# Kernel optimization log

Measured on AMD Instinct MI355X. Metric: run time of the kernel, lower is better.

Reference implementation:

```python
import jax, jax.numpy as jnp
import numpy as np

D_MODEL = 1024
D_CTRL = 1024
N_HEADS = 16
TOPK = 4
TEMPERATURE = 1.0
LN_EPS = 1e-5


def layer_norm(x, g, b):
    m = jnp.mean(x, axis=-1, keepdims=True)
    v = jnp.mean(jnp.square(x - m), axis=-1, keepdims=True)
    return (x - m) * jax.lax.rsqrt(v + LN_EPS) * g + b


def setup_inputs() -> dict:
    key = jax.random.key(0)
    ks = jax.random.split(key, 8)
    B, S = 8, 2048
    s = 0.02
    return {
        "x": jax.random.normal(ks[0], (B, S, D_MODEL), dtype=jnp.float32),
        "state": jnp.zeros((B, D_CTRL), dtype=jnp.float32),
        # pool LayerNorm
        "pool_g": jnp.ones((D_MODEL,), jnp.float32),
        "pool_b": jnp.zeros((D_MODEL,), jnp.float32),
        # inp_proj
        "inp_w": jax.random.normal(ks[1], (D_MODEL, D_CTRL), jnp.float32) * s,
        "inp_b": jnp.zeros((D_CTRL,), jnp.float32),
        # W_z, W_h
        "wz_w": jax.random.normal(ks[2], (D_CTRL, D_CTRL), jnp.float32) * s,
        "wz_b": jnp.zeros((D_CTRL,), jnp.float32),
        "wh_w": jax.random.normal(ks[3], (D_CTRL, D_CTRL), jnp.float32) * s,
        "wh_b": jnp.zeros((D_CTRL,), jnp.float32),
        # ln_h
        "lnh_g": jnp.ones((D_CTRL,), jnp.float32),
        "lnh_b": jnp.zeros((D_CTRL,), jnp.float32),
        # router: LayerNorm(d_model+d_ctrl) -> Linear -> GELU -> Linear
        "rln_g": jnp.ones((D_MODEL + D_CTRL,), jnp.float32),
        "rln_b": jnp.zeros((D_MODEL + D_CTRL,), jnp.float32),
        "r_w1": jax.random.normal(ks[4], (D_MODEL + D_CTRL, D_CTRL), jnp.float32) * s,
        "r_b1": jnp.zeros((D_CTRL,), jnp.float32),
        "r_w2": jax.random.normal(ks[5], (D_CTRL, N_HEADS), jnp.float32) * s,
        "r_b2": jnp.zeros((N_HEADS,), jnp.float32),
    }


def reference(x, state, pool_g, pool_b, inp_w, inp_b, wz_w, wz_b, wh_w, wh_b,
              lnh_g, lnh_b, rln_g, rln_b, r_w1, r_b1, r_w2, r_b2):
    B, S, D = x.shape
    # pool: LayerNorm over tokens then mean over sequence -> [B, d_model]
    g = jnp.mean(layer_norm(x, pool_g, pool_b), axis=1)
    x_ctrl = g @ inp_w + inp_b  # [B, d_ctrl]
    z = jax.nn.sigmoid(x_ctrl @ wz_w + wz_b)
    h_cand = jnp.tanh(x_ctrl @ wh_w + wh_b)
    h_new = (1.0 - z) * state + z * h_cand
    h_new = layer_norm(h_new, lnh_g, lnh_b)  # [B, d_ctrl]
    # token-conditioned router on concat([X, h_tok])
    h_tok = jnp.broadcast_to(h_new[:, None, :], (B, S, D_CTRL))
    cat = jnp.concatenate([x, h_tok], axis=-1)  # [B, S, d_model+d_ctrl]
    hid = jax.nn.gelu(layer_norm(cat, rln_g, rln_b) @ r_w1 + r_b1, approximate=False)
    logits = hid @ r_w2 + r_b2  # [B, S, H]
    alpha = jax.nn.softmax(logits / TEMPERATURE, axis=-1)
    # top-k mask + renorm
    _, topi = jax.lax.top_k(alpha, TOPK)  # [B, S, k]
    mask = jnp.sum(jax.nn.one_hot(topi, N_HEADS, dtype=alpha.dtype), axis=-2)  # [B, S, H]
    masked = alpha * mask
    denom = jnp.maximum(jnp.sum(masked, axis=-1, keepdims=True), 1e-12)
    alpha = masked / denom
    entropy = -jnp.mean(jnp.sum(alpha * jnp.log(jnp.maximum(alpha, 1e-12)), axis=-1))
    return (alpha, h_new, entropy)
```

## Files before the change

kernel.cpp:

```cpp
#include <hip/hip_runtime.h>
#include <hip/hip_bf16.h>
#include <math.h>

typedef unsigned short u16;
typedef __attribute__((ext_vector_type(8))) short bf16x8;
typedef __attribute__((ext_vector_type(4))) float f32x4;
typedef __attribute__((ext_vector_type(4))) unsigned short u16x4;

#define B_ 8
#define S_ 2048
#define T_ 16384
#define D_ 1024
#define H_ 16
#define EPS_ 1e-5f

__device__ __forceinline__ u16 f2bf(float f) {
    __hip_bfloat16 h = __float2bfloat16(f);
    union { __hip_bfloat16 h; u16 u; } cv; cv.h = h; return cv.u;
}
__device__ __forceinline__ float bf2f(u16 u) {
    union { u16 u; __hip_bfloat16 h; } cv; cv.u = u; return __bfloat162float(cv.h);
}

__global__ __launch_bounds__(256) void k01(const float* __restrict__ x,
        u16* __restrict__ xhi, u16* __restrict__ xlo,
        float* __restrict__ sx, float* __restrict__ sxx, float* __restrict__ gpart,
        const float* __restrict__ rw1, const float* __restrict__ rlng,
        const float* __restrict__ rlnb, u16* __restrict__ whiT, u16* __restrict__ wloT,
        float* __restrict__ c1part, float* __restrict__ c2part) {
    __shared__ float lacc[4][1024];
    __shared__ float ld[64][65];
    __shared__ float red[2][4][64];
    int blk = blockIdx.x;
    int tid = threadIdx.x;
    if (blk < 256) {
        int b = blk >> 5, chunk = blk & 31;
        int w = tid >> 6, lane = tid & 63;
        float acc[4][4];
        #pragma unroll
        for (int j = 0; j < 4; ++j)
            #pragma unroll
            for (int c = 0; c < 4; ++c) acc[j][c] = 0.f;
        for (int i = 0; i < 16; ++i) {
            int s = chunk * 64 + i * 4 + w;
            size_t tok = (size_t)b * S_ + s;
            size_t base = tok * D_;
            float4 v[4];
            float sum = 0.f, ssq = 0.f;
            #pragma unroll
            for (int j = 0; j < 4; ++j) {
                v[j] = *(const float4*)&x[base + j * 256 + lane * 4];
                sum += v[j].x + v[j].y + v[j].z + v[j].w;
                ssq += v[j].x * v[j].x + v[j].y * v[j].y + v[j].z * v[j].z + v[j].w * v[j].w;
            }
            #pragma unroll
            for (int m = 1; m < 64; m <<= 1) { sum += __shfl_xor(sum, m); ssq += __shfl_xor(ssq, m); }
            float mean = sum * (1.f / 1024.f);
            float var = ssq * (1.f / 1024.f) - mean * mean;
            float rstd = rsqrtf(var + EPS_);
            if (lane == 0) { sx[tok] = sum; sxx[tok] = ssq; }
            #pragma unroll
            for (int j = 0; j < 4; ++j) {
                float xs[4] = { v[j].x, v[j].y, v[j].z, v[j].w };
                u16 hs[4], ls[4];
                #pragma unroll
                for (int c = 0; c < 4; ++c) {
                    acc[j][c] += (xs[c] - mean) * rstd;
                    u16 h = f2bf(xs[c]);
                    hs[c] = h;
                    ls[c] = f2bf(xs[c] - bf2f(h));
                }
                size_t o = base + j * 256 + lane * 4;
                *(u16x4*)&xhi[o] = (u16x4){ hs[0], hs[1], hs[2], hs[3] };
                *(u16x4*)&xlo[o] = (u16x4){ ls[0], ls[1], ls[2], ls[3] };
            }
        }
        #pragma unroll
        for (int j = 0; j < 4; ++j)
            #pragma unroll
            for (int c = 0; c < 4; ++c) lacc[w][j * 256 + lane * 4 + c] = acc[j][c];
        __syncthreads();
        for (int q = 0; q < 4; ++q) {
            int n = q * 256 + tid;
            gpart[((size_t)b * 32 + chunk) * 1024 + n] =
                lacc[0][n] + lacc[1][n] + lacc[2][n] + lacc[3][n];
        }
    } else {
        int idx = blk - 256;
        int nb = idx & 15, kb = idx >> 4;
        int nl = tid & 63, kq = tid >> 6;
        int n0 = nb * 64, k0 = kb * 64;
        float a1 = 0.f, a2 = 0.f;
        #pragma unroll
        for (int r = 0; r < 16; ++r) {
            int kl = r * 4 + kq;
            int k = k0 + kl, n = n0 + nl;
            float w0 = rw1[(size_t)k * 1024 + n];
            ld[kl][nl] = w0;
            a1 += rlng[k] * w0;
            a2 += rlnb[k] * w0;
        }
        red[0][kq][nl] = a1;
        red[1][kq][nl] = a2;
        __syncthreads();
        if (tid < 64) {
            c1part[(size_t)kb * 1024 + n0 + tid] = red[0][0][tid] + red[0][1][tid] + red[0][2][tid] + red[0][3][tid];
            c2part[(size_t)kb * 1024 + n0 + tid] = red[1][0][tid] + red[1][1][tid] + red[1][2][tid] + red[1][3][tid];
        }
        if (kb < 16) {
            #pragma unroll
            for (int r = 0; r < 16; ++r) {
                int nl2 = r * 4 + kq;
                int k = k0 + nl, n = n0 + nl2;
                float w0 = ld[nl][nl2] * rlng[k];
                u16 hi = f2bf(w0);
                float lo = w0 - bf2f(hi);
                whiT[(size_t)n * 1024 + k] = hi;
                wloT[(size_t)n * 1024 + k] = f2bf(lo);
            }
        }
    }
}

__global__ __launch_bounds__(256) void kB(const float* __restrict__ gpart,
        const float* __restrict__ pg, const float* __restrict__ pb,
        const float* __restrict__ W, float* __restrict__ part,
        const float* __restrict__ c1part, const float* __restrict__ c2part,
        const float* __restrict__ rb1, float* __restrict__ c1, float* __restrict__ dvec) {
    int blk = blockIdx.x, t = threadIdx.x;
    if (blk < 128) {
        int nBlk = blk & 3, ks = blk >> 2;
        int n = nBlk * 256 + t;
        int k0 = ks * 32;
        __shared__ float sg[8][32];
        {
            int b = t >> 5, k = t & 31;
            float s = 0.f;
            #pragma unroll 8
            for (int p = 0; p < 32; ++p) s += gpart[((size_t)b * 32 + p) * 1024 + k0 + k];
            sg[b][k] = s * (1.f / 2048.f) * pg[k0 + k] + pb[k0 + k];
        }
        __syncthreads();
        float acc[8] = {};
        #pragma unroll
        for (int k = 0; k < 32; ++k) {
            float wv = W[(size_t)(k0 + k) * 1024 + n];
            #pragma unroll
            for (int b = 0; b < 8; ++b) acc[b] += sg[b][k] * wv;
        }
        #pragma unroll
        for (int b = 0; b < 8; ++b)
            part[((size_t)ks * 8 + b) * 1024 + n] = acc[b];
    } else {
        int n = (blk - 128) * 256 + t;
        float s1 = 0.f, s2 = 0.f;
        for (int p = 0; p < 32; ++p) { s1 += c1part[p * 1024 + n]; s2 += c2part[p * 1024 + n]; }
        c1[n] = s1;
        dvec[n] = s2 + rb1[n];
    }
}

__global__ __launch_bounds__(256) void kgemv2_f(const float* __restrict__ partIn,
        const float* __restrict__ bias,
        const float* __restrict__ Wz, const float* __restrict__ Wh,
        float* __restrict__ zpart, float* __restrict__ hpart) {
    int t = threadIdx.x;
    int n = blockIdx.x * 256 + t;
    int k0 = blockIdx.y * 32;
    __shared__ float sg[8][32];
    {
        int b = t >> 5, k = t & 31;
        float s = bias[k0 + k];
        #pragma unroll 8
        for (int p = 0; p < 32; ++p) s += partIn[((size_t)p * 8 + b) * 1024 + k0 + k];
        sg[b][k] = s;
    }
    __syncthreads();
    float az[8] = {}, ah[8] = {};
    #pragma unroll
    for (int k = 0; k < 32; ++k) {
        size_t o = (size_t)(k0 + k) * 1024 + n;
        float wz = Wz[o];
        float wh = Wh[o];
        #pragma unroll
        for (int b = 0; b < 8; ++b) { az[b] += sg[b][k] * wz; ah[b] += sg[b][k] * wh; }
    }
    #pragma unroll
    for (int b = 0; b < 8; ++b) {
        size_t o = ((size_t)blockIdx.y * 8 + b) * 1024 + n;
        zpart[o] = az[b];
        hpart[o] = ah[b];
    }
}

__global__ __launch_bounds__(256) void k3b_red_ln(const float* __restrict__ zpart,
        const float* __restrict__ hpart, const float* __restrict__ bz,
        const float* __restrict__ bh, const float* __restrict__ state,
        const float* __restrict__ lg, const float* __restrict__ lb,
        float* __restrict__ hnew, float* __restrict__ outh,
        float* __restrict__ shb, float* __restrict__ shhb) {
    int b = blockIdx.x, tid = threadIdx.x;
    int w = tid >> 6, lane = tid & 63;
    __shared__ float rbuf[4][2];
    float hp[4];
    float sum = 0.f, ssq = 0.f;
    #pragma unroll
    for (int q = 0; q < 4; ++q) {
        int n = q * 256 + tid;
        float az = bz[n], ah = bh[n];
        #pragma unroll 8
        for (int p = 0; p < 32; ++p) {
            size_t o = ((size_t)p * 8 + b) * 1024 + n;
            az += zpart[o];
            ah += hpart[o];
        }
        float z = 1.f / (1.f + expf(-az));
        float hc = tanhf(ah);
        float v = (1.f - z) * state[(size_t)b * 1024 + n] + z * hc;
        hp[q] = v; sum += v; ssq += v * v;
    }
    #pragma unroll
    for (int m = 1; m < 64; m <<= 1) { sum += __shfl_xor(sum, m); ssq += __shfl_xor(ssq, m); }
    if (lane == 0) { rbuf[w][0] = sum; rbuf[w][1] = ssq; }
    __syncthreads();
    sum = rbuf[0][0] + rbuf[1][0] + rbuf[2][0] + rbuf[3][0];
    ssq = rbuf[0][1] + rbuf[1][1] + rbuf[2][1] + rbuf[3][1];
    float mean = sum * (1.f / 1024.f);
    float var = ssq * (1.f / 1024.f) - mean * mean;
    float rstd = rsqrtf(var + EPS_);
    float s2 = 0.f, q2 = 0.f;
    #pragma unroll
    for (int q = 0; q < 4; ++q) {
        int n = q * 256 + tid;
        float h = (hp[q] - mean) * rstd * lg[n] + lb[n];
        hnew[(size_t)b * 1024 + n] = h;
        outh[(size_t)b * 1024 + n] = h;
        s2 += h; q2 += h * h;
    }
    #pragma unroll
    for (int m = 1; m < 64; m <<= 1) { s2 += __shfl_xor(s2, m); q2 += __shfl_xor(q2, m); }
    __syncthreads();
    if (lane == 0) { rbuf[w][0] = s2; rbuf[w][1] = q2; }
    __syncthreads();
    if (tid == 0) {
        shb[b] = rbuf[0][0] + rbuf[1][0] + rbuf[2][0] + rbuf[3][0];
        shhb[b] = rbuf[0][1] + rbuf[1][1] + rbuf[2][1] + rbuf[3][1];
    }
}

__global__ __launch_bounds__(256) void kE(const float* __restrict__ in,
        const float* __restrict__ W, const float* __restrict__ scale,
        float* __restrict__ part,
        const float* __restrict__ sx, const float* __restrict__ sxx,
        const float* __restrict__ shb, const float* __restrict__ shhb,
        float* __restrict__ pt, float* __restrict__ qt) {
    int blk = blockIdx.x, t = threadIdx.x;
    if (blk < 128) {
        int nBlk = blk & 3, ks = blk >> 2;
        int n = nBlk * 256 + t;
        int k0 = ks * 32;
        __shared__ float sg[8][32];
        {
            int b = t >> 5, k = t & 31;
            sg[b][k] = in[b * 1024 + k0 + k] * scale[k0 + k];
        }
        __syncthreads();
        float acc[8] = {};
        #pragma unroll
        for (int k = 0; k < 32; ++k) {
            float wv = W[(size_t)(k0 + k) * 1024 + n];
            #pragma unroll
            for (int b = 0; b < 8; ++b) acc[b] += sg[b][k] * wv;
        }
        #pragma unroll
        for (int b = 0; b < 8; ++b)
            part[((size_t)ks * 8 + b) * 1024 + n] = acc[b];
    } else {
        int tok = (blk - 128) * 256 + t;
        int b = tok >> 11;
        float m = (sx[tok] + shb[b]) * (1.f / 2048.f);
        float var = (sxx[tok] + shhb[b]) * (1.f / 2048.f) - m * m;
        float rstd = rsqrtf(var + EPS_);
        pt[tok] = rstd;
        qt[tok] = -m * rstd;
    }
}

__global__ __launch_bounds__(256) void kF(const float* __restrict__ part,
        float* __restrict__ vmat) {
    int i = blockIdx.x * 256 + threadIdx.x;
    int b = i >> 10, n = i & 1023;
    float s = 0.f;
    #pragma unroll 8
    for (int p = 0; p < 32; ++p) s += part[((size_t)p * 8 + b) * 1024 + n];
    vmat[i] = s;
}

__device__ __forceinline__ void gl16(const void* g, void* l) {
    __builtin_amdgcn_global_load_lds((const __attribute__((address_space(1))) void*)g,
                                     (__attribute__((address_space(3))) void*)l, 16, 0, 0);
}

__global__ __launch_bounds__(256, 1) void k5_gemm(
        const u16* __restrict__ xhi, const u16* __restrict__ xlo,
        const u16* __restrict__ whiT, const u16* __restrict__ wloT,
        const float* __restrict__ pt, const float* __restrict__ qt,
        const float* __restrict__ vmat, const float* __restrict__ c1,
        const float* __restrict__ dvec, const float* __restrict__ rw2,
        float* __restrict__ lpart) {
    __shared__ unsigned char smem[66048];
    u16* sAh = (u16*)smem;
    u16* sAl = sAh + 128 * 64;
    u16* sBh = sAl + 128 * 64;
    u16* sBl = sBh + 128 * 64;
    float* shid = (float*)smem;

    int bid = blockIdx.x;
    int x8 = bid & 7, j = bid >> 3;
    int mb = x8 * 16 + (j >> 3);
    int nb = j & 7;
    int tid = threadIdx.x;
    int lane = tid & 63, wid = tid >> 6;
    int wm = wid >> 1, wn = wid & 1;
    int l16 = lane & 15, lq = lane >> 4;

    f32x4 acc[4][4] = {};

    size_t aBase = (size_t)mb * 128 * 1024;
    size_t bBase = (size_t)nb * 128 * 1024;

    for (int kb = 0; kb < 16; ++kb) {
        __syncthreads();
        #pragma unroll
        for (int i = 0; i < 4; ++i) {
            int chunk = tid + 256 * i;
            int row = chunk >> 3, c8 = chunk & 7;
            int s8 = c8 ^ (row & 7);
            size_t go = (size_t)row * 1024 + (size_t)kb * 64 + s8 * 8;
            int lo = chunk * 16;
            gl16(xhi + aBase + go, (char*)sAh + lo);
            gl16(xlo + aBase + go, (char*)sAl + lo);
            gl16(whiT + bBase + go, (char*)sBh + lo);
            gl16(wloT + bBase + go, (char*)sBl + lo);
        }
        asm volatile("s_waitcnt vmcnt(0)" ::: "memory");
        __syncthreads();
        #pragma unroll
        for (int kk = 0; kk < 2; ++kk) {
            bf16x8 ah[4], al[4], bh[4], bl[4];
            int sl = ((kk * 4 + lq) ^ (l16 & 7)) * 8;
            #pragma unroll
            for (int f = 0; f < 4; ++f) {
                int ar = wm * 64 + f * 16 + l16;
                int br = wn * 64 + f * 16 + l16;
                ah[f] = *(const bf16x8*)&sAh[ar * 64 + sl];
                al[f] = *(const bf16x8*)&sAl[ar * 64 + sl];
                bh[f] = *(const bf16x8*)&sBh[br * 64 + sl];
                bl[f] = *(const bf16x8*)&sBl[br * 64 + sl];
            }
            #pragma unroll
            for (int mf = 0; mf < 4; ++mf)
                #pragma unroll
                for (int nf = 0; nf < 4; ++nf) {
                    acc[mf][nf] = __builtin_amdgcn_mfma_f32_16x16x32_bf16(ah[mf], bh[nf], acc[mf][nf], 0, 0, 0);
                    acc[mf][nf] = __builtin_amdgcn_mfma_f32_16x16x32_bf16(ah[mf], bl[nf], acc[mf][nf], 0, 0, 0);
                    acc[mf][nf] = __builtin_amdgcn_mfma_f32_16x16x32_bf16(al[mf], bh[nf], acc[mf][nf], 0, 0, 0);
                }
        }
    }
    __syncthreads();

    int token0 = mb * 128;
    int bidx = token0 >> 11;
    const float* vrow = vmat + (size_t)bidx * 1024;
    float vn[4], c1n[4], dn[4];
    #pragma unroll
    for (int nf = 0; nf < 4; ++nf) {
        int n = nb * 128 + wn * 64 + nf * 16 + l16;
        vn[nf] = vrow[n]; c1n[nf] = c1[n]; dn[nf] = dvec[n];
    }
    #pragma unroll
    for (int mf = 0; mf < 4; ++mf) {
        #pragma unroll
        for (int r = 0; r < 4; ++r) {
            int rowl = wm * 64 + mf * 16 + lq * 4 + r;
            float p = pt[token0 + rowl];
            float q = qt[token0 + rowl];
            #pragma unroll
            for (int nf = 0; nf < 4; ++nf) {
                int coll = wn * 64 + nf * 16 + l16;
                float pre = p * (acc[mf][nf][r] + vn[nf]) + q * c1n[nf] + dn[nf];
                float hid = 0.5f * pre * (1.f + erff(pre * 0.70710678118f));
                shid[rowl * 129 + coll] = hid;
            }
        }
    }
    __syncthreads();

    int r2 = tid >> 1, half = tid & 1;
    const float* w2b = rw2 + (size_t)nb * 128 * 16 + half * 8;
    float a8[8];
    #pragma unroll
    for (int h = 0; h < 8; ++h) a8[h] = 0.f;
    #pragma unroll 8
    for (int j2 = 0; j2 < 128; ++j2) {
        float hv = shid[r2 * 129 + j2];
        float4 w0 = *(const float4*)(w2b + (size_t)j2 * 16);
        float4 w1 = *(const float4*)(w2b + (size_t)j2 * 16 + 4);
        a8[0] += hv * w0.x; a8[1] += hv * w0.y; a8[2] += hv * w0.z; a8[3] += hv * w0.w;
        a8[4] += hv * w1.x; a8[5] += hv * w1.y; a8[6] += hv * w1.z; a8[7] += hv * w1.w;
    }
    float* lp = lpart + ((size_t)nb * T_ + token0 + r2) * 16 + half * 8;
    #pragma unroll
    for (int h = 0; h < 8; ++h) lp[h] = a8[h];
}

__global__ __launch_bounds__(256) void k6(const float* __restrict__ lpart,
        const float* __restrict__ rb2, float* __restrict__ alpha_out,
        float* __restrict__ entpart) {
    int blk = blockIdx.x;
    int tid = threadIdx.x;
    int token = blk * 16 + (tid >> 4);
    int h = tid & 15;
    float lg = rb2[h];
    #pragma unroll
    for (int p = 0; p < 8; ++p) lg += lpart[((size_t)p * T_ + token) * 16 + h];

    float mx = lg;
    #pragma unroll
    for (int m = 1; m < 16; m <<= 1) mx = fmaxf(mx, __shfl_xor(mx, m));
    float e = expf(lg - mx);
    float sum = e;
    #pragma unroll
    for (int m = 1; m < 16; m <<= 1) sum += __shfl_xor(sum, m);
    float a0 = e / sum;

    float work = lg;
    bool sel = false;
    #pragma unroll
    for (int it = 0; it < 4; ++it) {
        float bv = work; int bi = h;
        #pragma unroll
        for (int m = 1; m < 16; m <<= 1) {
            float ov = __shfl_xor(bv, m); int oi = __shfl_xor(bi, m);
            if (ov > bv || (ov == bv && oi < bi)) { bv = ov; bi = oi; }
        }
        if (h == bi) { sel = true; work = -1e30f; }
    }
    float am = sel ? a0 : 0.f;
    float den = am;
    #pragma unroll
    for (int m = 1; m < 16; m <<= 1) den += __shfl_xor(den, m);
    den = fmaxf(den, 1e-12f);
    float a = am / den;
    alpha_out[(size_t)token * 16 + h] = a;

    float term = a * logf(fmaxf(a, 1e-12f));
    #pragma unroll
    for (int m = 1; m < 64; m <<= 1) term += __shfl_xor(term, m);
    __shared__ float tw[4];
    if ((tid & 63) == 0) tw[tid >> 6] = term;
    __syncthreads();
    if (tid == 0) entpart[blk] = tw[0] + tw[1] + tw[2] + tw[3];
}

__global__ __launch_bounds__(256) void k7(const float* __restrict__ entpart,
        float* __restrict__ out_ent) {
    int tid = threadIdx.x;
    float s = 0.f;
    for (int i = tid; i < 1024; i += 256) s += entpart[i];
    #pragma unroll
    for (int m = 1; m < 64; m <<= 1) s += __shfl_xor(s, m);
    __shared__ float tw[4];
    if ((tid & 63) == 0) tw[tid >> 6] = s;
    __syncthreads();
    if (tid == 0) out_ent[0] = -(tw[0] + tw[1] + tw[2] + tw[3]) * (1.f / (float)T_);
}

extern "C" void kernel_launch(void* const* d_in, const int* in_sizes, int n_in,
                              void* d_out, int out_size, void* d_ws, size_t ws_size,
                              hipStream_t stream) {
    const float* x     = (const float*)d_in[0];
    const float* state = (const float*)d_in[1];
    const float* pg    = (const float*)d_in[2];
    const float* pbv   = (const float*)d_in[3];
    const float* inpw  = (const float*)d_in[4];
    const float* inpb  = (const float*)d_in[5];
    const float* wzw   = (const float*)d_in[6];
    const float* wzb   = (const float*)d_in[7];
    const float* whw   = (const float*)d_in[8];
    const float* whb   = (const float*)d_in[9];
    const float* lnhg  = (const float*)d_in[10];
    const float* lnhb  = (const float*)d_in[11];
    const float* rlng  = (const float*)d_in[12];
    const float* rlnb  = (const float*)d_in[13];
    const float* rw1   = (const float*)d_in[14];
    const float* rb1   = (const float*)d_in[15];
    const float* rw2   = (const float*)d_in[16];
    const float* rb2   = (const float*)d_in[17];
    float* out = (float*)d_out;
    (void)in_sizes; (void)n_in; (void)out_size; (void)ws_size;

    char* base = (char*)d_ws;
    size_t off = 0;
    auto alloc = [&](size_t bytes) -> char* {
        char* p = base + off;
        off = (off + bytes + 255) & ~(size_t)255;
        return p;
    };
    u16*   xhi    = (u16*)alloc((size_t)T_ * D_ * 2);
    u16*   xlo    = (u16*)alloc((size_t)T_ * D_ * 2);
    u16*   whiT   = (u16*)alloc((size_t)D_ * D_ * 2);
    u16*   wloT   = (u16*)alloc((size_t)D_ * D_ * 2);
    float* c1part = (float*)alloc(32 * 1024 * 4);
    float* c2part = (float*)alloc(32 * 1024 * 4);
    float* c1     = (float*)alloc(1024 * 4);
    float* dvec   = (float*)alloc(1024 * 4);
    float* sx     = (float*)alloc((size_t)T_ * 4);
    float* sxx    = (float*)alloc((size_t)T_ * 4);
    float* ptv    = (float*)alloc((size_t)T_ * 4);
    float* qtv    = (float*)alloc((size_t)T_ * 4);
    float* gpart  = (float*)alloc((size_t)8 * 32 * 1024 * 4);
    float* hnew   = (float*)alloc(8 * 1024 * 4);
    float* vmat   = (float*)alloc(8 * 1024 * 4);
    float* shb    = (float*)alloc(256);
    float* shhb   = (float*)alloc(256);
    float* lpart  = (float*)alloc((size_t)8 * T_ * H_ * 4);
    float* entpart= (float*)alloc(1024 * 4);
    float* partA  = (float*)alloc((size_t)32 * 8 * 1024 * 4);
    float* partB  = (float*)alloc((size_t)32 * 8 * 1024 * 4);
    float* partC  = (float*)alloc((size_t)32 * 8 * 1024 * 4);

    k01<<<768, 256, 0, stream>>>(x, xhi, xlo, sx, sxx, gpart,
                                 rw1, rlng, rlnb, whiT, wloT, c1part, c2part);
    kB<<<132, 256, 0, stream>>>(gpart, pg, pbv, inpw, partA,
                                c1part, c2part, rb1, c1, dvec);
    kgemv2_f<<<dim3(4, 32), 256, 0, stream>>>(partA, inpb, wzw, whw, partB, partC);
    k3b_red_ln<<<8, 256, 0, stream>>>(partB, partC, wzb, whb, state, lnhg, lnhb,
                                      hnew, out + (size_t)T_ * H_, shb, shhb);
    kE<<<192, 256, 0, stream>>>(hnew, rw1 + (size_t)1024 * 1024, rlng + 1024, partA,
                                sx, sxx, shb, shhb, ptv, qtv);
    kF<<<32, 256, 0, stream>>>(partA, vmat);
    k5_gemm<<<1024, 256, 0, stream>>>(xhi, xlo, whiT, wloT, ptv, qtv, vmat,
                                      c1, dvec, rw2, lpart);
    k6<<<1024, 256, 0, stream>>>(lpart, rb2, out, entpart);
    k7<<<1, 256, 0, stream>>>(entpart, out + (size_t)T_ * H_ + (size_t)B_ * D_);
}
```

Before: 193.9 us.

## Fuse small GEMV chain kernels into one cooperative kernel with grid syncs

Replaces five sequential small kernels (pooled GEMV, Wz/Wh GEMV, GRU-style update with LayerNorm, router GEMV on the hidden state, partial reduction) with one cooperative launch of 192 blocks, separated by grid-wide barriers. This removes per-launch overhead and the inter-kernel gaps on a latency-bound chain of tiny kernels. In exchange, each stage is bounded by grid.sync cost, blocks sit idle in the stages that use only a few of them, and the kernel now depends on cooperative launch support.

```diff
diff --git a/kernel.cpp b/kernel.cpp
--- a/kernel.cpp
+++ b/kernel.cpp
@@ -1,6 +1,9 @@
 #include <hip/hip_runtime.h>
 #include <hip/hip_bf16.h>
+#include <hip/hip_cooperative_groups.h>
 #include <math.h>
+
+namespace cg = cooperative_groups;
 
 typedef unsigned short u16;
 typedef __attribute__((ext_vector_type(8))) short bf16x8;
@@ -122,17 +125,30 @@
     }
 }
 
-__global__ __launch_bounds__(256) void kB(const float* __restrict__ gpart,
-        const float* __restrict__ pg, const float* __restrict__ pb,
-        const float* __restrict__ W, float* __restrict__ part,
+__global__ __launch_bounds__(256) void kChain(
+        const float* __restrict__ gpart, const float* __restrict__ pg,
+        const float* __restrict__ pb, const float* __restrict__ inpw,
+        float* __restrict__ partA,
         const float* __restrict__ c1part, const float* __restrict__ c2part,
-        const float* __restrict__ rb1, float* __restrict__ c1, float* __restrict__ dvec) {
+        const float* __restrict__ rb1, float* __restrict__ c1, float* __restrict__ dvec,
+        const float* __restrict__ inpb, const float* __restrict__ wzw,
+        const float* __restrict__ whw, float* __restrict__ partB, float* __restrict__ partC,
+        const float* __restrict__ wzb, const float* __restrict__ whb,
+        const float* __restrict__ state, const float* __restrict__ lnhg,
+        const float* __restrict__ lnhb, float* __restrict__ hnew, float* __restrict__ outh,
+        float* __restrict__ shb, float* __restrict__ shhb,
+        const float* __restrict__ rw1k, const float* __restrict__ rlngk,
+        const float* __restrict__ sx, const float* __restrict__ sxx,
+        float* __restrict__ ptv, float* __restrict__ qtv, float* __restrict__ vmat) {
+    cg::grid_group grid = cg::this_grid();
     int blk = blockIdx.x, t = threadIdx.x;
+    __shared__ float sg[8][32];
+    __shared__ float rbuf[4][2];
+
     if (blk < 128) {
         int nBlk = blk & 3, ks = blk >> 2;
         int n = nBlk * 256 + t;
         int k0 = ks * 32;
-        __shared__ float sg[8][32];
         {
             int b = t >> 5, k = t & 31;
             float s = 0.f;
@@ -144,156 +160,141 @@
         float acc[8] = {};
         #pragma unroll
         for (int k = 0; k < 32; ++k) {
-            float wv = W[(size_t)(k0 + k) * 1024 + n];
+            float wv = inpw[(size_t)(k0 + k) * 1024 + n];
             #pragma unroll
             for (int b = 0; b < 8; ++b) acc[b] += sg[b][k] * wv;
         }
         #pragma unroll
         for (int b = 0; b < 8; ++b)
-            part[((size_t)ks * 8 + b) * 1024 + n] = acc[b];
-    } else {
+            partA[((size_t)ks * 8 + b) * 1024 + n] = acc[b];
+    } else if (blk < 132) {
         int n = (blk - 128) * 256 + t;
         float s1 = 0.f, s2 = 0.f;
         for (int p = 0; p < 32; ++p) { s1 += c1part[p * 1024 + n]; s2 += c2part[p * 1024 + n]; }
         c1[n] = s1;
         dvec[n] = s2 + rb1[n];
     }
-}
-
-__global__ __launch_bounds__(256) void kgemv2_f(const float* __restrict__ partIn,
-        const float* __restrict__ bias,
-        const float* __restrict__ Wz, const float* __restrict__ Wh,
-        float* __restrict__ zpart, float* __restrict__ hpart) {
-    int t = threadIdx.x;
-    int n = blockIdx.x * 256 + t;
-    int k0 = blockIdx.y * 32;
-    __shared__ float sg[8][32];
-    {
-        int b = t >> 5, k = t & 31;
-        float s = bias[k0 + k];
-        #pragma unroll 8
-        for (int p = 0; p < 32; ++p) s += partIn[((size_t)p * 8 + b) * 1024 + k0 + k];
-        sg[b][k] = s;
-    }
-    __syncthreads();
-    float az[8] = {}, ah[8] = {};
-    #pragma unroll
-    for (int k = 0; k < 32; ++k) {
-        size_t o = (size_t)(k0 + k) * 1024 + n;
-        float wz = Wz[o];
-        float wh = Wh[o];
-        #pragma unroll
-        for (int b = 0; b < 8; ++b) { az[b] += sg[b][k] * wz; ah[b] += sg[b][k] * wh; }
-    }
-    #pragma unroll
-    for (int b = 0; b < 8; ++b) {
-        size_t o = ((size_t)blockIdx.y * 8 + b) * 1024 + n;
-        zpart[o] = az[b];
-        hpart[o] = ah[b];
-    }
-}
-
-__global__ __launch_bounds__(256) void k3b_red_ln(const float* __restrict__ zpart,
-        const float* __restrict__ hpart, const float* __restrict__ bz,
-        const float* __restrict__ bh, const float* __restrict__ state,
-        const float* __restrict__ lg, const float* __restrict__ lb,
-        float* __restrict__ hnew, float* __restrict__ outh,
-        float* __restrict__ shb, float* __restrict__ shhb) {
-    int b = blockIdx.x, tid = threadIdx.x;
-    int w = tid >> 6, lane = tid & 63;
-    __shared__ float rbuf[4][2];
-    float hp[4];
-    float sum = 0.f, ssq = 0.f;
-    #pragma unroll
-    for (int q = 0; q < 4; ++q) {
-        int n = q * 256 + tid;
-        float az = bz[n], ah = bh[n];
-        #pragma unroll 8
-        for (int p = 0; p < 32; ++p) {
-            size_t o = ((size_t)p * 8 + b) * 1024 + n;
-            az += zpart[o];
-            ah += hpart[o];
-        }
-        float z = 1.f / (1.f + expf(-az));
-        float hc = tanhf(ah);
-        float v = (1.f - z) * state[(size_t)b * 1024 + n] + z * hc;
-        hp[q] = v; sum += v; ssq += v * v;
-    }
-    #pragma unroll
-    for (int m = 1; m < 64; m <<= 1) { sum += __shfl_xor(sum, m); ssq += __shfl_xor(ssq, m); }
-    if (lane == 0) { rbuf[w][0] = sum; rbuf[w][1] = ssq; }
-    __syncthreads();
-    sum = rbuf[0][0] + rbuf[1][0] + rbuf[2][0] + rbuf[3][0];
-    ssq = rbuf[0][1] + rbuf[1][1] + rbuf[2][1] + rbuf[3][1];
-    float mean = sum * (1.f / 1024.f);
-    float var = ssq * (1.f / 1024.f) - mean * mean;
-    float rstd = rsqrtf(var + EPS_);
-    float s2 = 0.f, q2 = 0.f;
-    #pragma unroll
-    for (int q = 0; q < 4; ++q) {
-        int n = q * 256 + tid;
-        float h = (hp[q] - mean) * rstd * lg[n] + lb[n];
-        hnew[(size_t)b * 1024 + n] = h;
-        outh[(size_t)b * 1024 + n] = h;
-        s2 += h; q2 += h * h;
-    }
-    #pragma unroll
-    for (int m = 1; m < 64; m <<= 1) { s2 += __shfl_xor(s2, m); q2 += __shfl_xor(q2, m); }
-    __syncthreads();
-    if (lane == 0) { rbuf[w][0] = s2; rbuf[w][1] = q2; }
-    __syncthreads();
-    if (tid == 0) {
-        shb[b] = rbuf[0][0] + rbuf[1][0] + rbuf[2][0] + rbuf[3][0];
-        shhb[b] = rbuf[0][1] + rbuf[1][1] + rbuf[2][1] + rbuf[3][1];
-    }
-}
-
-__global__ __launch_bounds__(256) void kE(const float* __restrict__ in,
-        const float* __restrict__ W, const float* __restrict__ scale,
-        float* __restrict__ part,
-        const float* __restrict__ sx, const float* __restrict__ sxx,
-        const float* __restrict__ shb, const float* __restrict__ shhb,
-        float* __restrict__ pt, float* __restrict__ qt) {
-    int blk = blockIdx.x, t = threadIdx.x;
+    grid.sync();
+
     if (blk < 128) {
         int nBlk = blk & 3, ks = blk >> 2;
         int n = nBlk * 256 + t;
         int k0 = ks * 32;
-        __shared__ float sg[8][32];
         {
             int b = t >> 5, k = t & 31;
-            sg[b][k] = in[b * 1024 + k0 + k] * scale[k0 + k];
+            float s = inpb[k0 + k];
+            #pragma unroll 8
+            for (int p = 0; p < 32; ++p) s += partA[((size_t)p * 8 + b) * 1024 + k0 + k];
+            sg[b][k] = s;
+        }
+        __syncthreads();
+        float az[8] = {}, ah[8] = {};
+        #pragma unroll
+        for (int k = 0; k < 32; ++k) {
+            size_t o = (size_t)(k0 + k) * 1024 + n;
+            float wz = wzw[o];
+            float wh = whw[o];
+            #pragma unroll
+            for (int b = 0; b < 8; ++b) { az[b] += sg[b][k] * wz; ah[b] += sg[b][k] * wh; }
+        }
+        #pragma unroll
+        for (int b = 0; b < 8; ++b) {
+            size_t o = ((size_t)ks * 8 + b) * 1024 + n;
+            partB[o] = az[b];
+            partC[o] = ah[b];
+        }
+    }
+    grid.sync();
+
+    if (blk < 8) {
+        int b = blk;
+        int w = t >> 6, lane = t & 63;
+        float hp[4];
+        float sum = 0.f, ssq = 0.f;
+        #pragma unroll
+        for (int q = 0; q < 4; ++q) {
+            int n = q * 256 + t;
+            float az = wzb[n], ah = whb[n];
+            #pragma unroll 8
+            for (int p = 0; p < 32; ++p) {
+                size_t o = ((size_t)p * 8 + b) * 1024 + n;
+                az += partB[o];
+                ah += partC[o];
+            }
+            float z = 1.f / (1.f + expf(-az));
+            float hc = tanhf(ah);
+            float v = (1.f - z) * state[(size_t)b * 1024 + n] + z * hc;
+            hp[q] = v; sum += v; ssq += v * v;
+        }
+        #pragma unroll
+        for (int m = 1; m < 64; m <<= 1) { sum += __shfl_xor(sum, m); ssq += __shfl_xor(ssq, m); }
+        if (lane == 0) { rbuf[w][0] = sum; rbuf[w][1] = ssq; }
+        __syncthreads();
+        sum = rbuf[0][0] + rbuf[1][0] + rbuf[2][0] + rbuf[3][0];
+        ssq = rbuf[0][1] + rbuf[1][1] + rbuf[2][1] + rbuf[3][1];
+        float mean = sum * (1.f / 1024.f);
+        float var = ssq * (1.f / 1024.f) - mean * mean;
+        float rstd = rsqrtf(var + EPS_);
+        float s2 = 0.f, q2 = 0.f;
+        #pragma unroll
+        for (int q = 0; q < 4; ++q) {
+            int n = q * 256 + t;
+            float h = (hp[q] - mean) * rstd * lnhg[n] + lnhb[n];
+            hnew[(size_t)b * 1024 + n] = h;
+            outh[(size_t)b * 1024 + n] = h;
+            s2 += h; q2 += h * h;
+        }
+        #pragma unroll
+        for (int m = 1; m < 64; m <<= 1) { s2 += __shfl_xor(s2, m); q2 += __shfl_xor(q2, m); }
+        __syncthreads();
+        if (lane == 0) { rbuf[w][0] = s2; rbuf[w][1] = q2; }
+        __syncthreads();
+        if (t == 0) {
+            shb[b] = rbuf[0][0] + rbuf[1][0] + rbuf[2][0] + rbuf[3][0];
+            shhb[b] = rbuf[0][1] + rbuf[1][1] + rbuf[2][1] + rbuf[3][1];
+        }
+    }
+    grid.sync();
+
+    if (blk < 128) {
+        int nBlk = blk & 3, ks = blk >> 2;
+        int n = nBlk * 256 + t;
+        int k0 = ks * 32;
+        __syncthreads();
+        {
+            int b = t >> 5, k = t & 31;
+            sg[b][k] = hnew[b * 1024 + k0 + k] * rlngk[k0 + k];
         }
         __syncthreads();
         float acc[8] = {};
         #pragma unroll
         for (int k = 0; k < 32; ++k) {
-            float wv = W[(size_t)(k0 + k) * 1024 + n];
+            float wv = rw1k[(size_t)(k0 + k) * 1024 + n];
             #pragma unroll
             for (int b = 0; b < 8; ++b) acc[b] += sg[b][k] * wv;
         }
         #pragma unroll
         for (int b = 0; b < 8; ++b)
-            part[((size_t)ks * 8 + b) * 1024 + n] = acc[b];
+            partA[((size_t)ks * 8 + b) * 1024 + n] = acc[b];
     } else {
         int tok = (blk - 128) * 256 + t;
         int b = tok >> 11;
         float m = (sx[tok] + shb[b]) * (1.f / 2048.f);
         float var = (sxx[tok] + shhb[b]) * (1.f / 2048.f) - m * m;
         float rstd = rsqrtf(var + EPS_);
-        pt[tok] = rstd;
-        qt[tok] = -m * rstd;
-    }
-}
-
-__global__ __launch_bounds__(256) void kF(const float* __restrict__ part,
-        float* __restrict__ vmat) {
-    int i = blockIdx.x * 256 + threadIdx.x;
-    int b = i >> 10, n = i & 1023;
-    float s = 0.f;
-    #pragma unroll 8
-    for (int p = 0; p < 32; ++p) s += part[((size_t)p * 8 + b) * 1024 + n];
-    vmat[i] = s;
+        ptv[tok] = rstd;
+        qtv[tok] = -m * rstd;
+    }
+    grid.sync();
+
+    if (blk < 32) {
+        int i = blk * 256 + t;
+        int b = i >> 10, n = i & 1023;
+        float s = 0.f;
+        #pragma unroll 8
+        for (int p = 0; p < 32; ++p) s += partA[((size_t)p * 8 + b) * 1024 + n];
+        vmat[i] = s;
+    }
 }
 
 __device__ __forceinline__ void gl16(const void* g, void* l) {
@@ -531,18 +532,30 @@
     float* partB  = (float*)alloc((size_t)32 * 8 * 1024 * 4);
     float* partC  = (float*)alloc((size_t)32 * 8 * 1024 * 4);
 
+    float* outh   = out + (size_t)T_ * H_;
+    float* outent = out + (size_t)T_ * H_ + (size_t)B_ * D_;
+    const float* rw1k  = rw1 + (size_t)1024 * 1024;
+    const float* rlngk = rlng + 1024;
+
     k01<<<768, 256, 0, stream>>>(x, xhi, xlo, sx, sxx, gpart,
                                  rw1, rlng, rlnb, whiT, wloT, c1part, c2part);
-    kB<<<132, 256, 0, stream>>>(gpart, pg, pbv, inpw, partA,
-                                c1part, c2part, rb1, c1, dvec);
-    kgemv2_f<<<dim3(4, 32), 256, 0, stream>>>(partA, inpb, wzw, whw, partB, partC);
-    k3b_red_ln<<<8, 256, 0, stream>>>(partB, partC, wzb, whb, state, lnhg, lnhb,
-                                      hnew, out + (size_t)T_ * H_, shb, shhb);
-    kE<<<192, 256, 0, stream>>>(hnew, rw1 + (size_t)1024 * 1024, rlng + 1024, partA,
-                                sx, sxx, shb, shhb, ptv, qtv);
-    kF<<<32, 256, 0, stream>>>(partA, vmat);
+
+    {
+        void* args[] = {
+            (void*)&gpart, (void*)&pg, (void*)&pbv, (void*)&inpw, (void*)&partA,
+            (void*)&c1part, (void*)&c2part, (void*)&rb1, (void*)&c1, (void*)&dvec,
+            (void*)&inpb, (void*)&wzw, (void*)&whw, (void*)&partB, (void*)&partC,
+            (void*)&wzb, (void*)&whb, (void*)&state, (void*)&lnhg, (void*)&lnhb,
+            (void*)&hnew, (void*)&outh, (void*)&shb, (void*)&shhb,
+            (void*)&rw1k, (void*)&rlngk, (void*)&sx, (void*)&sxx,
+            (void*)&ptv, (void*)&qtv, (void*)&vmat
+        };
+        hipLaunchCooperativeKernel((const void*)kChain, dim3(192), dim3(256),
+                                   args, 0, stream);
+    }
+
     k5_gemm<<<1024, 256, 0, stream>>>(xhi, xlo, whiT, wloT, ptv, qtv, vmat,
                                       c1, dvec, rw2, lpart);
     k6<<<1024, 256, 0, stream>>>(lpart, rb2, out, entpart);
-    k7<<<1, 256, 0, stream>>>(entpart, out + (size_t)T_ * H_ + (size_t)B_ * D_);
-}
+    k7<<<1, 256, 0, stream>>>(entpart, outent);
+}
```

Result: slower. 292.1 us (+50.7%).
